# Kernel tuning notes

Measured on AMD Instinct MI355X. Metric: run time of the kernel, lower is better.

## Reference

```python
import jax, jax.numpy as jnp
import numpy as np

B, S, E, H = 2, 2048, 1024, 16
DH = E // H  # 64
FF = 4 * E


def setup_inputs() -> dict:
    key = jax.random.key(0)
    ks = jax.random.split(key, 13)
    s = 0.02
    return {
        "x": jax.random.normal(ks[0], (B, S, E), dtype=jnp.float32),
        "Wq": jax.random.normal(ks[1], (H, E, DH), dtype=jnp.float32) * s,
        "Wk": jax.random.normal(ks[2], (H, E, DH), dtype=jnp.float32) * s,
        "Wv": jax.random.normal(ks[3], (H, E, DH), dtype=jnp.float32) * s,
        "Wo": jax.random.normal(ks[4], (E, E), dtype=jnp.float32) * s,
        "bo": jnp.zeros((E,), dtype=jnp.float32),
        "W1": jax.random.normal(ks[5], (E, FF), dtype=jnp.float32) * s,
        "b1": jnp.zeros((FF,), dtype=jnp.float32),
        "W2": jax.random.normal(ks[6], (FF, E), dtype=jnp.float32) * s,
        "b2": jnp.zeros((E,), dtype=jnp.float32),
        "g1": jnp.ones((E,), dtype=jnp.float32),
        "beta1": jnp.zeros((E,), dtype=jnp.float32),
        "g2": jnp.ones((E,), dtype=jnp.float32),
        "beta2": jnp.zeros((E,), dtype=jnp.float32),
    }


def _layernorm(x, g, b, eps=1e-5):
    mu = jnp.mean(x, axis=-1, keepdims=True)
    var = jnp.var(x, axis=-1, keepdims=True)
    return (x - mu) * jax.lax.rsqrt(var + eps) * g + b


def reference(x, Wq, Wk, Wv, Wo, bo, W1, b1, W2, b2, g1, beta1, g2, beta2):
    # Pre-LN attention (dropout is identity in eval mode)
    nx = _layernorm(x, g1, beta1)
    # per-head projections, batched over heads: [B,H,S,DH]
    q = jnp.einsum('bse,hed->bhsd', nx, Wq)
    k = jnp.einsum('bse,hed->bhsd', nx, Wk)
    v = jnp.einsum('bse,hed->bhsd', nx, Wv)
    scores = jnp.einsum('bhqd,bhkd->bhqk', q, k) * (DH ** -0.5)  # [B,H,S,S]
    seq = x.shape[1]
    causal = jnp.tril(jnp.ones((seq, seq), dtype=bool))
    scores = jnp.where(causal, scores, -jnp.inf)
    w = jax.nn.softmax(scores, axis=-1)
    attn = jnp.einsum('bhqk,bhkd->bhqd', w, v)  # [B,H,S,DH]
    # concat heads (head order matches ModuleList cat order)
    attn = attn.transpose(0, 2, 1, 3).reshape(x.shape[0], seq, E)
    attn_out = attn @ Wo + bo
    x = x + attn_out
    # FFN
    nx2 = _layernorm(x, g2, beta2)
    ffn = jax.nn.relu(nx2 @ W1 + b1) @ W2 + b2
    return x + ffn
```

## Files before the change

kernel.cpp:

```cpp
#include <hip/hip_runtime.h>


typedef __attribute__((ext_vector_type(8))) short short8;
typedef __attribute__((ext_vector_type(4))) float floatx4;

__device__ inline unsigned short f32_to_bf16(float f) {
  unsigned u = __float_as_uint(f);
  unsigned rb = (u >> 16) & 1u;
  u += 0x7fffu + rb;
  return (unsigned short)(u >> 16);
}
__device__ inline unsigned f32_to_bf16_hi(float f) {
  return (__float_as_uint(f) + 0x8000u) >> 16;
}
__device__ inline float bf16_to_f32(unsigned short u) {
  return __uint_as_float(((unsigned)u) << 16);
}

__device__ inline void gload16(const void* g, void* l) {
  __builtin_amdgcn_global_load_lds(
      (const __attribute__((address_space(1))) void*)g,
      (__attribute__((address_space(3))) void*)l, 16, 0, 0);
}

__global__ __launch_bounds__(256) void transpose_to_bf16(
    const float* __restrict__ in, unsigned short* __restrict__ out,
    int R, int C, int ldo, long in_bs, long out_bs) {
  __shared__ float tile[32][33];
  in  += (size_t)blockIdx.z * in_bs;
  out += (size_t)blockIdx.z * out_bs;
  const int c0 = blockIdx.x * 32, r0 = blockIdx.y * 32;
  const int tx = threadIdx.x & 31, ty = threadIdx.x >> 5;
#pragma unroll
  for (int i = 0; i < 32; i += 8)
    tile[ty + i][tx] = in[(size_t)(r0 + ty + i) * C + c0 + tx];
  __syncthreads();
#pragma unroll
  for (int i = 0; i < 32; i += 8)
    out[(size_t)(c0 + ty + i) * ldo + r0 + tx] = f32_to_bf16(tile[tx][ty + i]);
}

__global__ __launch_bounds__(256) void transpose_qkv_to_bf16(
    const float* __restrict__ Wq, const float* __restrict__ Wk,
    const float* __restrict__ Wv, unsigned short* __restrict__ out) {
  __shared__ float tile[32][33];
  const int z = blockIdx.z, m = z >> 4;
  const float* in = (m == 0 ? Wq : (m == 1 ? Wk : Wv)) + (size_t)(z & 15) * 65536;
  unsigned short* o = out + (size_t)z * 65536;
  const int c0 = blockIdx.x * 32, r0 = blockIdx.y * 32;
  const int tx = threadIdx.x & 31, ty = threadIdx.x >> 5;
#pragma unroll
  for (int i = 0; i < 32; i += 8)
    tile[ty + i][tx] = in[(size_t)(r0 + ty + i) * 64 + c0 + tx];
  __syncthreads();
#pragma unroll
  for (int i = 0; i < 32; i += 8)
    o[(size_t)(c0 + ty + i) * 1024 + r0 + tx] = f32_to_bf16(tile[tx][ty + i]);
}

__global__ __launch_bounds__(256) void transpose_v(
    const unsigned short* __restrict__ qkv, unsigned short* __restrict__ vT) {
  __shared__ unsigned short tile[32][33];
  const int bh = blockIdx.z, b = bh >> 4, h = bh & 15;
  const int k0 = blockIdx.x * 32, d0 = blockIdx.y * 32;
  const int tx = threadIdx.x & 31, ty = threadIdx.x >> 5;
#pragma unroll
  for (int i = 0; i < 32; i += 8)
    tile[ty + i][tx] = qkv[(size_t)(b * 2048 + k0 + ty + i) * 3072 + 2048 + h * 64 + d0 + tx];
  __syncthreads();
#pragma unroll
  for (int i = 0; i < 32; i += 8)
    vT[((size_t)bh * 64 + d0 + ty + i) * 2048 + k0 + tx] = tile[tx][ty + i];
}

__global__ __launch_bounds__(256) void layernorm_bf16(
    const float* __restrict__ x, const float* __restrict__ g,
    const float* __restrict__ be, unsigned short* __restrict__ out) {
  const int row = blockIdx.x;
  const int t = threadIdx.x;
  floatx4 v = ((const floatx4*)(x + (size_t)row * 1024))[t];
  float s  = v[0] + v[1] + v[2] + v[3];
  float s2 = v[0]*v[0] + v[1]*v[1] + v[2]*v[2] + v[3]*v[3];
#pragma unroll
  for (int off = 1; off < 64; off <<= 1) {
    s  += __shfl_xor(s, off);
    s2 += __shfl_xor(s2, off);
  }
  __shared__ float red[8];
  const int wave = t >> 6, lane = t & 63;
  if (lane == 0) { red[wave] = s; red[wave + 4] = s2; }
  __syncthreads();
  float ts  = red[0] + red[1] + red[2] + red[3];
  float ts2 = red[4] + red[5] + red[6] + red[7];
  float mu  = ts * (1.f / 1024.f);
  float var = ts2 * (1.f / 1024.f) - mu * mu;
  float rs  = rsqrtf(var + 1e-5f);
  floatx4 gv = ((const floatx4*)g)[t];
  floatx4 bv = ((const floatx4*)be)[t];
  ushort4 ov;
  ov.x = f32_to_bf16((v[0] - mu) * rs * gv[0] + bv[0]);
  ov.y = f32_to_bf16((v[1] - mu) * rs * gv[1] + bv[1]);
  ov.z = f32_to_bf16((v[2] - mu) * rs * gv[2] + bv[2]);
  ov.w = f32_to_bf16((v[3] - mu) * rs * gv[3] + bv[3]);
  ((ushort4*)(out + (size_t)row * 1024))[t] = ov;
}

__global__ __launch_bounds__(256, 4) void gemm_bf16(
    const unsigned short* __restrict__ A, const unsigned short* __restrict__ Bt,
    const float* __restrict__ bias, const float* __restrict__ resid,
    void* __restrict__ Cout, int M, int N, int Kfull, int Klen, int mode) {
  __shared__ unsigned short As[2][128 * 32];
  __shared__ unsigned short Bs[2][128 * 32];
  const int t = threadIdx.x;
  const int NB = gridDim.x;
  const int bid = blockIdx.y * NB + blockIdx.x;
  const int xcd = bid & 7, slot = bid >> 3;
  const int m0 = (xcd * 4 + slot / NB) * 128;
  const int n0 = (slot % NB) * 128;
  const int koff = blockIdx.z * Klen;
  const int lane = t & 63, wave = t >> 6;
  const int wm = (wave >> 1) * 64, wn = (wave & 1) * 64;
  const int l15 = lane & 15, quad = lane >> 4;

  floatx4 acc[4][4];
#pragma unroll
  for (int i = 0; i < 4; ++i)
#pragma unroll
    for (int j = 0; j < 4; ++j) acc[i][j] = floatx4{0.f, 0.f, 0.f, 0.f};

  const int srow = wave * 32 + (lane >> 2);
  const int scol = (lane & 3) * 8;
  const unsigned short* Ag0 = A + (size_t)(m0 + srow) * Kfull + koff + scol;
  const unsigned short* Ag1 = Ag0 + (size_t)16 * Kfull;
  const unsigned short* Bg0 = Bt + (size_t)(n0 + srow) * Kfull + koff + scol;
  const unsigned short* Bg1 = Bg0 + (size_t)16 * Kfull;
  const int sbase0 = (wave * 2 + 0) * 512;
  const int sbase1 = (wave * 2 + 1) * 512;

  const int KT = Klen >> 5;
  gload16(Ag0, &As[0][sbase0]);
  gload16(Ag1, &As[0][sbase1]);
  gload16(Bg0, &Bs[0][sbase0]);
  gload16(Bg1, &Bs[0][sbase1]);

  int buf = 0;
  for (int kt = 0; kt < KT; ++kt) {
    if (kt + 1 < KT) {
      const int ko = (kt + 1) * 32;
      gload16(Ag0 + ko, &As[buf ^ 1][sbase0]);
      gload16(Ag1 + ko, &As[buf ^ 1][sbase1]);
      gload16(Bg0 + ko, &Bs[buf ^ 1][sbase0]);
      gload16(Bg1 + ko, &Bs[buf ^ 1][sbase1]);
      asm volatile("s_waitcnt vmcnt(4)" ::: "memory");
    } else {
      asm volatile("s_waitcnt vmcnt(0)" ::: "memory");
    }
    __builtin_amdgcn_s_barrier();
    short8 a[4], b[4];
#pragma unroll
    for (int i = 0; i < 4; ++i)
      a[i] = *(const short8*)&As[buf][(wm + i * 16 + l15) * 32 + quad * 8];
#pragma unroll
    for (int i = 0; i < 4; ++i)
      b[i] = *(const short8*)&Bs[buf][(wn + i * 16 + l15) * 32 + quad * 8];
#pragma unroll
    for (int i = 0; i < 4; ++i)
#pragma unroll
      for (int j = 0; j < 4; ++j)
        acc[i][j] = __builtin_amdgcn_mfma_f32_16x16x32_bf16(a[i], b[j], acc[i][j], 0, 0, 0);
    __builtin_amdgcn_s_barrier();
    buf ^= 1;
  }
  __builtin_amdgcn_sched_barrier(0);

  if (mode == 0 || mode == 2) {
    unsigned short* Cs = &As[0][0];
#pragma unroll
    for (int p = 0; p < 2; ++p) {
      if ((wm >> 6) == p) {
#pragma unroll
        for (int i = 0; i < 4; ++i)
#pragma unroll
          for (int j = 0; j < 4; ++j)
#pragma unroll
            for (int r = 0; r < 4; ++r) {
              const int rl = i * 16 + quad * 4 + r;
              float v = acc[i][j][r];
              if (mode == 2) {
                v += bias[n0 + wn + j * 16 + l15];
                v = fmaxf(v, 0.f);
              }
              Cs[rl * 128 + wn + j * 16 + l15] = f32_to_bf16(v);
            }
      }
      __syncthreads();
#pragma unroll
      for (int c = 0; c < 4; ++c) {
        const int idx = c * 256 + t;
        const int row = idx >> 4, chunk = idx & 15;
        *(uint4*)&((unsigned short*)Cout)[(size_t)(m0 + p * 64 + row) * N + n0 + chunk * 8] =
            *(const uint4*)&Cs[row * 128 + chunk * 8];
      }
      __syncthreads();
    }
  } else {
    const size_t poff = (size_t)blockIdx.z * 4096 * 1024;
#pragma unroll
    for (int i = 0; i < 4; ++i)
#pragma unroll
      for (int j = 0; j < 4; ++j) {
        const int col = n0 + wn + j * 16 + l15;
        const int rb = m0 + wm + i * 16 + quad * 4;
#pragma unroll
        for (int r = 0; r < 4; ++r) {
          const int row = rb + r;
          float v = acc[i][j][r];
          if (mode == 1) {
            v += bias[col] + resid[(size_t)row * N + col];
            ((float*)Cout)[(size_t)row * N + col] = v;
          } else {
            ((float*)Cout)[poff + (size_t)row * N + col] = v;
          }
        }
      }
  }
}

__global__ __launch_bounds__(256) void splitk_reduce(
    const float* __restrict__ p, const float* __restrict__ bias,
    const float* __restrict__ resid, float* __restrict__ out) {
  const int t = threadIdx.x;
  const size_t base = (size_t)blockIdx.x * 256 + t;
  floatx4 a = ((const floatx4*)p)[base];
  floatx4 b = ((const floatx4*)p)[1048576 + base];
  floatx4 rv = ((const floatx4*)resid)[base];
  floatx4 bv = ((const floatx4*)bias)[t];
  ((floatx4*)out)[base] = a + b + rv + bv;
}

__global__ __launch_bounds__(256) void splitk_reduce_ln(
    const float* __restrict__ p, const float* __restrict__ bias,
    const float* __restrict__ resid, const float* __restrict__ g,
    const float* __restrict__ be, float* __restrict__ xout,
    unsigned short* __restrict__ nxout) {
  const int row = blockIdx.x, t = threadIdx.x;
  const size_t base = (size_t)row * 256 + t;
  floatx4 a = ((const floatx4*)p)[base];
  floatx4 b = ((const floatx4*)p)[1048576 + base];
  floatx4 rv = ((const floatx4*)resid)[base];
  floatx4 bv = ((const floatx4*)bias)[t];
  floatx4 v = a + b + rv + bv;
  ((floatx4*)xout)[base] = v;
  float s  = v[0] + v[1] + v[2] + v[3];
  float s2 = v[0]*v[0] + v[1]*v[1] + v[2]*v[2] + v[3]*v[3];
#pragma unroll
  for (int off = 1; off < 64; off <<= 1) {
    s  += __shfl_xor(s, off);
    s2 += __shfl_xor(s2, off);
  }
  __shared__ float red[8];
  const int wave = t >> 6, lane = t & 63;
  if (lane == 0) { red[wave] = s; red[wave + 4] = s2; }
  __syncthreads();
  float ts  = red[0] + red[1] + red[2] + red[3];
  float ts2 = red[4] + red[5] + red[6] + red[7];
  float mu  = ts * (1.f / 1024.f);
  float var = ts2 * (1.f / 1024.f) - mu * mu;
  float rs  = rsqrtf(var + 1e-5f);
  floatx4 gv = ((const floatx4*)g)[t];
  floatx4 bev = ((const floatx4*)be)[t];
  ushort4 ov;
  ov.x = f32_to_bf16((v[0] - mu) * rs * gv[0] + bev[0]);
  ov.y = f32_to_bf16((v[1] - mu) * rs * gv[1] + bev[1]);
  ov.z = f32_to_bf16((v[2] - mu) * rs * gv[2] + bev[2]);
  ov.w = f32_to_bf16((v[3] - mu) * rs * gv[3] + bev[3]);
  ((ushort4*)(nxout + (size_t)row * 1024))[t] = ov;
}

__global__ __launch_bounds__(256, 3) void flash_attn_mfma(
    const unsigned short* __restrict__ qkv,
    const unsigned short* __restrict__ vT,
    unsigned short* __restrict__ attn) {
  const int id = blockIdx.x;
  const int xcd = id & 7, slot = id >> 3;
  const int bh = xcd * 4 + (slot & 3);
  const int qt = 15 - (slot >> 2);
  const int b = bh >> 4, h = bh & 15;
  const int q0 = qt * 128;
  const int t = threadIdx.x;
  const int wave = t >> 6, lane = t & 63;
  const int l15 = lane & 15, quad = lane >> 4;

  __shared__ unsigned short Ks[2][64][68];
  __shared__ unsigned short Vs[2][64][68];
  __shared__ unsigned short Ps[4][32][68];

  const size_t qbase = (size_t)b * 2048 * 3072;
  const int qrow_w = q0 + wave * 32;
  const unsigned short* Kbase = qkv + qbase + 1024 + h * 64;
  const unsigned short* Vbase = vT + (size_t)bh * 64 * 2048;

  short8 qf[2][2];
#pragma unroll
  for (int mf = 0; mf < 2; ++mf)
#pragma unroll
    for (int kc = 0; kc < 2; ++kc) {
      short8 raw = *(const short8*)(qkv + qbase +
          (size_t)(qrow_w + mf * 16 + l15) * 3072 + h * 64 + kc * 32 + quad * 8);
      short8 sc;
#pragma unroll
      for (int j = 0; j < 8; ++j)
        sc[j] = (short)f32_to_bf16(bf16_to_f32((unsigned short)raw[j]) * 0.125f);
      qf[mf][kc] = sc;
    }

  floatx4 o[2][4];
  float l_s[2] = {0.f, 0.f};
#pragma unroll
  for (int mf = 0; mf < 2; ++mf)
#pragma unroll
    for (int jd = 0; jd < 4; ++jd) o[mf][jd] = floatx4{0.f, 0.f, 0.f, 0.f};

  const int sr = t >> 3, so = (t & 7) * 8;

  uint4 kr0 = *(const uint4*)(Kbase + (size_t)sr * 3072 + so);
  uint4 kr1 = *(const uint4*)(Kbase + (size_t)(sr + 32) * 3072 + so);
  uint4 vr0 = *(const uint4*)(Vbase + (size_t)sr * 2048 + so);
  uint4 vr1 = *(const uint4*)(Vbase + (size_t)(sr + 32) * 2048 + so);

  const int ntiles = 2 * qt + 2;
  int buf = 0;
  for (int kt = 0; kt < ntiles; ++kt) {
    const int k0 = kt * 64;
    *(uint4*)&Ks[buf][sr][so]      = kr0;
    *(uint4*)&Ks[buf][sr + 32][so] = kr1;
    *(uint4*)&Vs[buf][sr][so]      = vr0;
    *(uint4*)&Vs[buf][sr + 32][so] = vr1;
    if (kt + 1 < ntiles) {
      const int k1 = k0 + 64;
      kr0 = *(const uint4*)(Kbase + (size_t)(k1 + sr) * 3072 + so);
      kr1 = *(const uint4*)(Kbase + (size_t)(k1 + sr + 32) * 3072 + so);
      vr0 = *(const uint4*)(Vbase + (size_t)sr * 2048 + k1 + so);
      vr1 = *(const uint4*)(Vbase + (size_t)(sr + 32) * 2048 + k1 + so);
    }
    asm volatile("s_waitcnt lgkmcnt(0)" ::: "memory");
    __builtin_amdgcn_s_barrier();

    if (k0 <= qrow_w + 31) {
      short8 kf[2][4];
#pragma unroll
      for (int kc = 0; kc < 2; ++kc)
#pragma unroll
        for (int jb = 0; jb < 4; ++jb)
          kf[kc][jb] = *(const short8*)&Ks[buf][jb * 16 + l15][kc * 32 + quad * 8];

      floatx4 st[2][4];
#pragma unroll
      for (int mf = 0; mf < 2; ++mf)
#pragma unroll
        for (int jb = 0; jb < 4; ++jb) st[mf][jb] = floatx4{0.f, 0.f, 0.f, 0.f};
      __builtin_amdgcn_s_setprio(1);
#pragma unroll
      for (int kc = 0; kc < 2; ++kc)
#pragma unroll
        for (int jb = 0; jb < 4; ++jb) {
#pragma unroll
          for (int mf = 0; mf < 2; ++mf)
            st[mf][jb] = __builtin_amdgcn_mfma_f32_16x16x32_bf16(
                kf[kc][jb], qf[mf][kc], st[mf][jb], 0, 0, 0);
        }
      __builtin_amdgcn_s_setprio(0);

#pragma unroll
      for (int mf = 0; mf < 2; ++mf) {
        const int qq = qrow_w + mf * 16 + l15;
#pragma unroll
        for (int jb = 0; jb < 4; ++jb) {
          const int keyb = k0 + jb * 16 + quad * 4;
          float p0 = (keyb + 0 > qq) ? 0.f : __expf(st[mf][jb][0]);
          float p1 = (keyb + 1 > qq) ? 0.f : __expf(st[mf][jb][1]);
          float p2 = (keyb + 2 > qq) ? 0.f : __expf(st[mf][jb][2]);
          float p3 = (keyb + 3 > qq) ? 0.f : __expf(st[mf][jb][3]);
          l_s[mf] += (p0 + p1) + (p2 + p3);
          uint2 pk;
          pk.x = (f32_to_bf16_hi(p1) << 16) | f32_to_bf16_hi(p0);
          pk.y = (f32_to_bf16_hi(p3) << 16) | f32_to_bf16_hi(p2);
          *(uint2*)&Ps[wave][mf * 16 + l15][jb * 16 + quad * 4] = pk;
        }
      }

      __builtin_amdgcn_s_setprio(1);
#pragma unroll
      for (int kc = 0; kc < 2; ++kc) {
        short8 pf0 = *(const short8*)&Ps[wave][l15][kc * 32 + quad * 8];
        short8 pf1 = *(const short8*)&Ps[wave][16 + l15][kc * 32 + quad * 8];
#pragma unroll
        for (int jd = 0; jd < 4; ++jd) {
          short8 vf = *(const short8*)&Vs[buf][jd * 16 + l15][kc * 32 + quad * 8];
          o[0][jd] = __builtin_amdgcn_mfma_f32_16x16x32_bf16(pf0, vf, o[0][jd], 0, 0, 0);
          o[1][jd] = __builtin_amdgcn_mfma_f32_16x16x32_bf16(pf1, vf, o[1][jd], 0, 0, 0);
        }
      }
      __builtin_amdgcn_s_setprio(0);
    }
    buf ^= 1;
  }

#pragma unroll
  for (int mf = 0; mf < 2; ++mf) {
    l_s[mf] += __shfl_xor(l_s[mf], 16);
    l_s[mf] += __shfl_xor(l_s[mf], 32);
  }

#pragma unroll
  for (int mf = 0; mf < 2; ++mf)
#pragma unroll
    for (int r = 0; r < 4; ++r) {
      const int qloc = quad * 4 + r;
      const float lsum = __shfl(l_s[mf], qloc);
      const float rl = 1.f / lsum;
      const int row = b * 2048 + q0 + wave * 32 + mf * 16 + qloc;
#pragma unroll
      for (int jd = 0; jd < 4; ++jd)
        attn[(size_t)row * 1024 + h * 64 + jd * 16 + l15] =
            f32_to_bf16(o[mf][jd][r] * rl);
    }
}

extern "C" void kernel_launch(void* const* d_in, const int* in_sizes, int n_in,
                              void* d_out, int out_size, void* d_ws, size_t ws_size,
                              hipStream_t stream) {
  const float* x   = (const float*)d_in[0];
  const float* Wq  = (const float*)d_in[1];
  const float* Wk  = (const float*)d_in[2];
  const float* Wv  = (const float*)d_in[3];
  const float* Wo  = (const float*)d_in[4];
  const float* bo  = (const float*)d_in[5];
  const float* W1  = (const float*)d_in[6];
  const float* b1  = (const float*)d_in[7];
  const float* W2  = (const float*)d_in[8];
  const float* b2  = (const float*)d_in[9];
  const float* g1  = (const float*)d_in[10];
  const float* be1 = (const float*)d_in[11];
  const float* g2  = (const float*)d_in[12];
  const float* be2 = (const float*)d_in[13];
  float* out = (float*)d_out;

  char* ws = (char*)d_ws;
  size_t off = 0;
  auto alloc = [&](size_t bytes) -> void* {
    void* p = ws + off;
    off += (bytes + 255) & ~(size_t)255;
    return p;
  };
  unsigned short* WqkvT = (unsigned short*)alloc(3072ull * 1024 * 2);
  unsigned short* WoT   = (unsigned short*)alloc(1024ull * 1024 * 2);
  unsigned short* W1T   = (unsigned short*)alloc(4096ull * 1024 * 2);
  unsigned short* W2T   = (unsigned short*)alloc(1024ull * 4096 * 2);
  unsigned short* nx    = (unsigned short*)alloc(4096ull * 1024 * 2);
  unsigned short* qkv   = (unsigned short*)alloc(4096ull * 3072 * 2);
  unsigned short* attn  = (unsigned short*)alloc(4096ull * 1024 * 2);
  float*          x1    = (float*)alloc(4096ull * 1024 * 4);
  unsigned short* nx2   = (unsigned short*)alloc(4096ull * 1024 * 2);
  unsigned short* hbuf  = (unsigned short*)alloc(4096ull * 4096 * 2);
  unsigned short* vT    = hbuf;
  float*          part  = (float*)nx;

  dim3 blk(256);
  transpose_qkv_to_bf16<<<dim3(2, 32, 48), blk, 0, stream>>>(Wq, Wk, Wv, WqkvT);
  transpose_to_bf16<<<dim3(32, 32, 1), blk, 0, stream>>>(Wo, WoT, 1024, 1024, 1024, 0, 0);
  transpose_to_bf16<<<dim3(128, 32, 1), blk, 0, stream>>>(W1, W1T, 1024, 4096, 1024, 0, 0);
  transpose_to_bf16<<<dim3(32, 128, 1), blk, 0, stream>>>(W2, W2T, 4096, 1024, 4096, 0, 0);

  layernorm_bf16<<<4096, blk, 0, stream>>>(x, g1, be1, nx);
  gemm_bf16<<<dim3(24, 32, 1), blk, 0, stream>>>(nx, WqkvT, nullptr, nullptr, qkv, 4096, 3072, 1024, 1024, 0);
  transpose_v<<<dim3(64, 2, 32), blk, 0, stream>>>(qkv, vT);
  flash_attn_mfma<<<dim3(512, 1, 1), blk, 0, stream>>>(qkv, vT, attn);
  gemm_bf16<<<dim3(8, 32, 2), blk, 0, stream>>>(attn, WoT, nullptr, nullptr, part, 4096, 1024, 1024, 512, 3);
  splitk_reduce_ln<<<4096, blk, 0, stream>>>(part, bo, x, g2, be2, x1, nx2);
  gemm_bf16<<<dim3(32, 32, 1), blk, 0, stream>>>(nx2, W1T, b1, nullptr, hbuf, 4096, 4096, 1024, 1024, 2);
  gemm_bf16<<<dim3(8, 32, 2), blk, 0, stream>>>(hbuf, W2T, nullptr, nullptr, part, 4096, 1024, 4096, 2048, 3);
  splitk_reduce<<<4096, blk, 0, stream>>>(part, b2, x1, out);
}
```

Baseline: 356.9 us.

## Add 256x256-tile 8-wave GEMM with swizzled LDS for QKV and FFN1

Introduces a new bf16 GEMM kernel using 256x256 output tiles, 512 threads, a BK of 64 with XOR-swizzled LDS layout, and staging of the next k-tile interleaved between MFMA compute phases with setprio hints. The QKV projection and FFN up-projection (bias+ReLU) now use it, and the old kernel's bf16 epilogue path is removed. The goal is higher arithmetic intensity and better latency hiding for the two large GEMMs. In exchange, the tile count is small (192/256 blocks) relative to the CU count, and register pressure from the 8x4 accumulators is high.

```diff
diff --git a/kernel.cpp b/kernel.cpp
--- a/kernel.cpp
+++ b/kernel.cpp
@@ -105,6 +105,119 @@
   ((ushort4*)(out + (size_t)row * 1024))[t] = ov;
 }
 
+#define STAGE_HALF(PTR, LDSARR, H, KTT)                                        \
+  {                                                                            \
+    gload16(PTR + (size_t)((H) * 128) * Kfull + (KTT) * 64,                    \
+            &LDSARR[(H) * 8192 + ldsb]);                                       \
+    gload16(PTR + (size_t)((H) * 128 + 8) * Kfull + (KTT) * 64,                \
+            &LDSARR[(H) * 8192 + ldsb + 512]);                                 \
+  }
+
+#define PHASE_COMPUTE(Q)                                                       \
+  {                                                                            \
+    short8 af[2][2];                                                           \
+    _Pragma("unroll") for (int ii = 0; ii < 2; ++ii)                           \
+      _Pragma("unroll") for (int kk = 0; kk < 2; ++kk)                         \
+        af[ii][kk] = *(const short8*)&As[s][(wm + ((Q) * 2 + ii) * 16 + l15) * 64 + \
+                                            (((kk * 4 + quad) ^ rsw) * 8)];    \
+    __builtin_amdgcn_s_setprio(1);                                             \
+    _Pragma("unroll") for (int ii = 0; ii < 2; ++ii)                           \
+      _Pragma("unroll") for (int j = 0; j < 4; ++j)                            \
+        _Pragma("unroll") for (int kk = 0; kk < 2; ++kk)                       \
+          acc[(Q) * 2 + ii][j] = __builtin_amdgcn_mfma_f32_16x16x32_bf16(      \
+              af[ii][kk], bfr[j][kk], acc[(Q) * 2 + ii][j], 0, 0, 0);          \
+    __builtin_amdgcn_s_setprio(0);                                             \
+  }
+
+__global__ __launch_bounds__(512, 2) void gemm256_bf16(
+    const unsigned short* __restrict__ A, const unsigned short* __restrict__ Bt,
+    const float* __restrict__ bias, unsigned short* __restrict__ Cout,
+    int M, int N, int Kfull, int mode) {
+  __shared__ unsigned short As[2][256 * 64];
+  __shared__ unsigned short Bs[2][256 * 64];
+  const int t = threadIdx.x;
+  const int lane = t & 63, wave = t >> 6;
+  const int l15 = lane & 15, quad = lane >> 4;
+  const int wm = (wave >> 2) * 128, wn = (wave & 3) * 64;
+  const int rsw = l15 & 7;
+
+  const int cpx = gridDim.x >> 3;
+  const int wgid = ((int)blockIdx.x & 7) * cpx + ((int)blockIdx.x >> 3);
+  const int NBN = N >> 8;
+  const int m0 = (wgid / NBN) << 8;
+  const int n0 = (wgid % NBN) << 8;
+
+  floatx4 acc[8][4];
+#pragma unroll
+  for (int i = 0; i < 8; ++i)
+#pragma unroll
+    for (int j = 0; j < 4; ++j) acc[i][j] = floatx4{0.f, 0.f, 0.f, 0.f};
+
+  const int rr = lane >> 3, cc7 = lane & 7;
+  const unsigned short* Ap = A + (size_t)(m0 + wave * 16 + rr) * Kfull + (cc7 ^ rr) * 8;
+  const unsigned short* Bp = Bt + (size_t)(n0 + wave * 16 + rr) * Kfull + (cc7 ^ rr) * 8;
+  const int ldsb = wave * 1024;
+
+  const int KT = Kfull >> 6;
+  STAGE_HALF(Ap, As[0], 0, 0)
+  STAGE_HALF(Ap, As[0], 1, 0)
+  STAGE_HALF(Bp, Bs[0], 0, 0)
+  STAGE_HALF(Bp, Bs[0], 1, 0)
+
+  for (int kt = 0; kt < KT; ++kt) {
+    const int s = kt & 1, sx = s ^ 1;
+    const bool st = (kt + 1 < KT);
+    if (st) {
+      STAGE_HALF(Ap, As[sx], 0, kt + 1)
+      asm volatile("s_waitcnt vmcnt(2)" ::: "memory");
+    } else {
+      asm volatile("s_waitcnt vmcnt(0)" ::: "memory");
+    }
+    __builtin_amdgcn_s_barrier();
+    short8 bfr[4][2];
+#pragma unroll
+    for (int j = 0; j < 4; ++j)
+#pragma unroll
+      for (int kk = 0; kk < 2; ++kk)
+        bfr[j][kk] = *(const short8*)&Bs[s][(wn + j * 16 + l15) * 64 +
+                                            (((kk * 4 + quad) ^ rsw) * 8)];
+    PHASE_COMPUTE(0)
+    if (st) STAGE_HALF(Ap, As[sx], 1, kt + 1)
+    PHASE_COMPUTE(1)
+    if (st) STAGE_HALF(Bp, Bs[sx], 0, kt + 1)
+    PHASE_COMPUTE(2)
+    if (st) STAGE_HALF(Bp, Bs[sx], 1, kt + 1)
+    PHASE_COMPUTE(3)
+    __builtin_amdgcn_s_barrier();
+  }
+  __builtin_amdgcn_sched_barrier(0);
+
+  float bv[4] = {0.f, 0.f, 0.f, 0.f};
+  if (mode) {
+#pragma unroll
+    for (int j = 0; j < 4; ++j) bv[j] = bias[n0 + wn + j * 16 + l15];
+  }
+  unsigned short* Cw = (wave < 4) ? (&As[0][0] + wave * 8192)
+                                  : (&Bs[0][0] + (wave - 4) * 8192);
+#pragma unroll
+  for (int i = 0; i < 8; ++i)
+#pragma unroll
+    for (int j = 0; j < 4; ++j)
+#pragma unroll
+      for (int r = 0; r < 4; ++r) {
+        float v = acc[i][j][r];
+        if (mode) v = fmaxf(v + bv[j], 0.f);
+        Cw[(i * 16 + quad * 4 + r) * 64 + j * 16 + l15] = f32_to_bf16(v);
+      }
+  unsigned short* Cg = Cout + (size_t)(m0 + wm) * N + n0 + wn;
+#pragma unroll
+  for (int c = 0; c < 16; ++c) {
+    const int idx = c * 64 + lane;
+    const int row = idx >> 3, c8 = idx & 7;
+    *(uint4*)&Cg[(size_t)row * N + c8 * 8] = *(const uint4*)&Cw[row * 64 + c8 * 8];
+  }
+}
+
 __global__ __launch_bounds__(256, 4) void gemm_bf16(
     const unsigned short* __restrict__ A, const unsigned short* __restrict__ Bt,
     const float* __restrict__ bias, const float* __restrict__ resid,
@@ -173,57 +286,25 @@
   }
   __builtin_amdgcn_sched_barrier(0);
 
-  if (mode == 0 || mode == 2) {
-    unsigned short* Cs = &As[0][0];
-#pragma unroll
-    for (int p = 0; p < 2; ++p) {
-      if ((wm >> 6) == p) {
-#pragma unroll
-        for (int i = 0; i < 4; ++i)
-#pragma unroll
-          for (int j = 0; j < 4; ++j)
-#pragma unroll
-            for (int r = 0; r < 4; ++r) {
-              const int rl = i * 16 + quad * 4 + r;
-              float v = acc[i][j][r];
-              if (mode == 2) {
-                v += bias[n0 + wn + j * 16 + l15];
-                v = fmaxf(v, 0.f);
-              }
-              Cs[rl * 128 + wn + j * 16 + l15] = f32_to_bf16(v);
-            }
-      }
-      __syncthreads();
-#pragma unroll
-      for (int c = 0; c < 4; ++c) {
-        const int idx = c * 256 + t;
-        const int row = idx >> 4, chunk = idx & 15;
-        *(uint4*)&((unsigned short*)Cout)[(size_t)(m0 + p * 64 + row) * N + n0 + chunk * 8] =
-            *(const uint4*)&Cs[row * 128 + chunk * 8];
-      }
-      __syncthreads();
-    }
-  } else {
-    const size_t poff = (size_t)blockIdx.z * 4096 * 1024;
-#pragma unroll
-    for (int i = 0; i < 4; ++i)
-#pragma unroll
-      for (int j = 0; j < 4; ++j) {
-        const int col = n0 + wn + j * 16 + l15;
-        const int rb = m0 + wm + i * 16 + quad * 4;
-#pragma unroll
-        for (int r = 0; r < 4; ++r) {
-          const int row = rb + r;
-          float v = acc[i][j][r];
-          if (mode == 1) {
-            v += bias[col] + resid[(size_t)row * N + col];
-            ((float*)Cout)[(size_t)row * N + col] = v;
-          } else {
-            ((float*)Cout)[poff + (size_t)row * N + col] = v;
-          }
+  const size_t poff = (size_t)blockIdx.z * 4096 * 1024;
+#pragma unroll
+  for (int i = 0; i < 4; ++i)
+#pragma unroll
+    for (int j = 0; j < 4; ++j) {
+      const int col = n0 + wn + j * 16 + l15;
+      const int rb = m0 + wm + i * 16 + quad * 4;
+#pragma unroll
+      for (int r = 0; r < 4; ++r) {
+        const int row = rb + r;
+        float v = acc[i][j][r];
+        if (mode == 1) {
+          v += bias[col] + resid[(size_t)row * N + col];
+          ((float*)Cout)[(size_t)row * N + col] = v;
+        } else {
+          ((float*)Cout)[poff + (size_t)row * N + col] = v;
         }
       }
-  }
+    }
 }
 
 __global__ __launch_bounds__(256) void splitk_reduce(
@@ -473,12 +554,12 @@
   transpose_to_bf16<<<dim3(32, 128, 1), blk, 0, stream>>>(W2, W2T, 4096, 1024, 4096, 0, 0);
 
   layernorm_bf16<<<4096, blk, 0, stream>>>(x, g1, be1, nx);
-  gemm_bf16<<<dim3(24, 32, 1), blk, 0, stream>>>(nx, WqkvT, nullptr, nullptr, qkv, 4096, 3072, 1024, 1024, 0);
+  gemm256_bf16<<<dim3(192), dim3(512), 0, stream>>>(nx, WqkvT, nullptr, qkv, 4096, 3072, 1024, 0);
   transpose_v<<<dim3(64, 2, 32), blk, 0, stream>>>(qkv, vT);
   flash_attn_mfma<<<dim3(512, 1, 1), blk, 0, stream>>>(qkv, vT, attn);
   gemm_bf16<<<dim3(8, 32, 2), blk, 0, stream>>>(attn, WoT, nullptr, nullptr, part, 4096, 1024, 1024, 512, 3);
   splitk_reduce_ln<<<4096, blk, 0, stream>>>(part, bo, x, g2, be2, x1, nx2);
-  gemm_bf16<<<dim3(32, 32, 1), blk, 0, stream>>>(nx2, W1T, b1, nullptr, hbuf, 4096, 4096, 1024, 1024, 2);
+  gemm256_bf16<<<dim3(256), dim3(512), 0, stream>>>(nx2, W1T, b1, hbuf, 4096, 4096, 1024, 1);
   gemm_bf16<<<dim3(8, 32, 2), blk, 0, stream>>>(hbuf, W2T, nullptr, nullptr, part, 4096, 1024, 4096, 2048, 3);
   splitk_reduce<<<4096, blk, 0, stream>>>(part, b2, x1, out);
 }
```

New measurement: 362.5 us. No clear change (+1.6%).
